# Optimization experiments

Hardware: AMD Instinct MI355X
Metric: run time of the kernel (lower is better)

Reference implementation:

```python
import jax, jax.numpy as jnp
from jax import lax
import numpy as np

N, L, C, G, K = 8, 4096, 256, 8, 3
GC = C // G
DILATION = 1
OFFSET_SCALE = 1.0
LN_EPS = 1e-6


def setup_inputs() -> dict:
    key = jax.random.key(0)
    ks = jax.random.split(key, 14)
    s = lambda k, shp, sc: jax.random.normal(k, shp, jnp.float32) * sc
    return {
        "x": jax.random.normal(ks[0], (N, L, C), jnp.float32),
        "W_in": s(ks[1], (C, C), (1.0 / C) ** 0.5),      # input_proj (in,out)
        "b_in": jnp.zeros((C,), jnp.float32),
        "conv_w": s(ks[2], (C, 1, K), 0.2),              # depthwise conv (O, I/g, K)
        "conv_b": jnp.zeros((C,), jnp.float32),
        "ln_g": jnp.ones((C,), jnp.float32),
        "ln_b": jnp.zeros((C,), jnp.float32),
        "W_off": s(ks[3], (C, G * K), 0.02),             # offset_linear
        "b_off": s(ks[4], (G * K,), 0.02),
        "W_mask": s(ks[5], (C, G * K), 0.02),            # mask_linear
        "b_mask": s(ks[6], (G * K,), 0.02),
        "W_out": s(ks[7], (C, C), (1.0 / C) ** 0.5),     # output_proj
        "b_out": jnp.zeros((C,), jnp.float32),
    }


def _dcnv3_1d(x, W_in, b_in, conv_w, conv_b, ln_g, ln_b,
              W_off, b_off, W_mask, b_mask, W_out, b_out):
    # x: (N, L, C)
    x_proj = x @ W_in + b_in                                     # (N,L,C)

    # depthwise conv -> LayerNorm(C) -> GELU  (the offset/mask feature branch)
    xc = x.transpose(0, 2, 1)                                    # (N,C,L)
    pad = (K - 1) // 2
    y = lax.conv_general_dilated(
        xc, conv_w, window_strides=(1,), padding=[(pad, pad)],
        dimension_numbers=("NCH", "OIH", "NCH"), feature_group_count=C)
    y = y + conv_b[None, :, None]
    y = y.transpose(0, 2, 1)                                     # (N,L,C)
    mu = y.mean(-1, keepdims=True)
    var = ((y - mu) ** 2).mean(-1, keepdims=True)
    y = (y - mu) * lax.rsqrt(var + LN_EPS) * ln_g + ln_b
    x_feat = jax.nn.gelu(y, approximate=False)                   # torch GELU = exact erf

    offset = (x_feat @ W_off + b_off).reshape(N, L, G, K)
    mask = jax.nn.softmax((x_feat @ W_mask + b_mask).reshape(N, L, G, K), axis=-1)

    # sampling locations (grid_sample with align_corners=True unnormalizes back to loc)
    ref_p = jnp.arange(L, dtype=jnp.float32)                     # (L,)
    lo = float(-((K - 1) // 2))
    hi = float((K - 1) // 2)
    dil_grid = jnp.linspace(lo, hi, K) * DILATION                # (K,)
    loc = ref_p[None, :, None, None] + dil_grid[None, None, None, :] \
          + offset * OFFSET_SCALE                                # (N,L,G,K)
    loc = jnp.remainder(loc, L)                                  # in [0, L)

    # bilinear sample along L with zero padding (matches F.grid_sample, H=1)
    f0 = jnp.floor(loc)
    w1 = loc - f0
    w0 = 1.0 - w1
    i0 = jnp.clip(f0.astype(jnp.int32), 0, L - 1)
    i1 = i0 + 1
    valid1 = (i1 < L)
    i1c = jnp.where(valid1, i1, 0)

    x_g = x_proj.reshape(N, L, G, GC)                            # (N,L,G,gc)
    nidx = jnp.arange(N)[:, None, None, None]
    gidx = jnp.arange(G)[None, None, :, None]
    v0 = x_g[nidx, i0, gidx]                                     # (N,L,G,K,gc)
    v1 = x_g[nidx, i1c, gidx] * valid1[..., None].astype(x_g.dtype)
    sampled = w0[..., None] * v0 + w1[..., None] * v1            # (N,L,G,K,gc)

    out = (sampled * mask[..., None]).sum(axis=3)                # (N,L,G,gc)
    out = out.reshape(N, L, C)
    return out @ W_out + b_out


def reference(x, W_in, b_in, conv_w, conv_b, ln_g, ln_b,
              W_off, b_off, W_mask, b_mask, W_out, b_out):
    return _dcnv3_1d(x, W_in, b_in, conv_w, conv_b, ln_g, ln_b,
                     W_off, b_off, W_mask, b_mask, W_out, b_out)
```

## Files before the change

kernel.cpp:

```cpp
#include <hip/hip_runtime.h>
#include <math.h>

constexpr int LL = 4096;
constexpr int CC = 256;
constexpr int MM = 32768;

typedef unsigned int u32;
typedef unsigned short u16;
typedef __attribute__((ext_vector_type(8))) short bf16x8;
typedef __attribute__((ext_vector_type(4))) float f32x4;

__device__ __forceinline__ u16 f2b(float f) {
    u32 u = __float_as_uint(f);
    u32 r = (u + 0x7fffu + ((u >> 16) & 1u)) >> 16;
    return (u16)r;
}

__device__ __forceinline__ void gl_lds16(const u16* g, u16* l) {
    __builtin_amdgcn_global_load_lds(
        (const __attribute__((address_space(1))) unsigned int*)g,
        (__attribute__((address_space(3))) unsigned int*)l, 16, 0, 0);
}

__global__ __launch_bounds__(256) void prep_w(
    const float* __restrict__ W_in, const float* __restrict__ W_out,
    const float* __restrict__ W_off, const float* __restrict__ W_mask,
    u16* __restrict__ Wt_in, u16* __restrict__ Wt_out, u16* __restrict__ Wcomb)
{
    const int b = blockIdx.x, t = threadIdx.x;
    if (b < 256) {
        Wt_in[b * 256 + t]  = f2b(W_in[t * 256 + b]);
        Wt_out[b * 256 + t] = f2b(W_out[t * 256 + b]);
    } else {
        const int j = b - 256;
        const float v = (j < 24) ? W_off[t * 24 + j] : W_mask[t * 24 + (j - 24)];
        Wcomb[j * 256 + t] = f2b(v);
    }
}

__global__ __launch_bounds__(256) void conv_ln_gelu(
    const float* __restrict__ x, const float* __restrict__ cw,
    const float* __restrict__ cbias, const float* __restrict__ lng,
    const float* __restrict__ lnb, u16* __restrict__ xf, u16* __restrict__ xb16)
{
    const int wave = threadIdx.x >> 6;
    const int lane = threadIdx.x & 63;
    const int nl = (blockIdx.x << 2) + wave;
    const int l = nl & (LL - 1);
    const int c0 = lane << 2;
    const size_t base = (size_t)nl * CC + c0;

    float4 xc = *(const float4*)&x[base];
    float4 xm = make_float4(0.f, 0.f, 0.f, 0.f);
    float4 xp = make_float4(0.f, 0.f, 0.f, 0.f);
    if (l > 0)      xm = *(const float4*)&x[base - CC];
    if (l < LL - 1) xp = *(const float4*)&x[base + CC];

    ushort4 xbv;
    xbv.x = f2b(xc.x); xbv.y = f2b(xc.y); xbv.z = f2b(xc.z); xbv.w = f2b(xc.w);
    *(ushort4*)&xb16[base] = xbv;

    float xmv[4] = {xm.x, xm.y, xm.z, xm.w};
    float xcv[4] = {xc.x, xc.y, xc.z, xc.w};
    float xpv[4] = {xp.x, xp.y, xp.z, xp.w};

    float y[4];
    float sum = 0.f, sq = 0.f;
#pragma unroll
    for (int j = 0; j < 4; ++j) {
        const int c = c0 + j;
        float v = fmaf(xmv[j], cw[c * 3 + 0],
                  fmaf(xcv[j], cw[c * 3 + 1],
                  fmaf(xpv[j], cw[c * 3 + 2], cbias[c])));
        y[j] = v;
        sum += v;
        sq  += v * v;
    }
#pragma unroll
    for (int off = 32; off > 0; off >>= 1) {
        sum += __shfl_xor(sum, off);
        sq  += __shfl_xor(sq, off);
    }
    const float mu  = sum * (1.f / CC);
    const float var = sq * (1.f / CC) - mu * mu;
    const float rs  = rsqrtf(var + 1e-6f);

    ushort4 o;
    float ov[4];
#pragma unroll
    for (int j = 0; j < 4; ++j) {
        const int c = c0 + j;
        const float tn = (y[j] - mu) * rs * lng[c] + lnb[c];
        ov[j] = 0.5f * tn * (1.f + erff(tn * 0.70710678118654752f));
    }
    o.x = f2b(ov[0]); o.y = f2b(ov[1]); o.z = f2b(ov[2]); o.w = f2b(ov[3]);
    *(ushort4*)&xf[base] = o;
}

__global__ __launch_bounds__(256, 3) void gemm1(
    const u16* __restrict__ xb, const u16* __restrict__ Wt_in,
    const float* __restrict__ b_in, u16* __restrict__ xprojb)
{
    __shared__ u16 As[2][128 * 32];
    __shared__ u16 Bs[2][128 * 32];

    const int t = threadIdx.x;
    const int w = t >> 6, lane = t & 63;
    const int lr = lane & 15, lk = lane >> 4;
    const int wm = w >> 1, wn = w & 1;

    const int d = blockIdx.x;
    const int m_t = (d & 7) * 32 + (d >> 4);
    const int n_t = (d >> 3) & 1;
    const int m0 = m_t * 128, n0 = n_t * 128;

    const int srow = lane >> 2;
    const int scol = (lane & 3) * 8;

    f32x4 acc[4][4];
#pragma unroll
    for (int i = 0; i < 4; ++i)
#pragma unroll
        for (int j = 0; j < 4; ++j) acc[i][j] = f32x4{0.f, 0.f, 0.f, 0.f};

    auto STAGE = [&](int buf, int kt) {
        const int k0 = kt * 32;
#pragma unroll
        for (int j = 0; j < 2; ++j) {
            const int rr = (w * 2 + j) * 16 + srow;
            u16* ldsbase_a = &As[buf][0] + (w * 2 + j) * 512;
            u16* ldsbase_b = &Bs[buf][0] + (w * 2 + j) * 512;
            gl_lds16(xb    + ((size_t)(m0 + rr) << 8) + k0 + scol, ldsbase_a);
            gl_lds16(Wt_in + ((size_t)(n0 + rr) << 8) + k0 + scol, ldsbase_b);
        }
    };

    STAGE(0, 0);
    for (int kt = 0; kt < 8; ++kt) {
        const int cur = kt & 1;
        __syncthreads();
        if (kt < 7) STAGE(cur ^ 1, kt + 1);
        bf16x8 af[4], bfr[4];
#pragma unroll
        for (int mt = 0; mt < 4; ++mt)
            af[mt] = *(const bf16x8*)&As[cur][(wm * 64 + mt * 16 + lr) * 32 + lk * 8];
#pragma unroll
        for (int nt = 0; nt < 4; ++nt)
            bfr[nt] = *(const bf16x8*)&Bs[cur][(wn * 64 + nt * 16 + lr) * 32 + lk * 8];
#pragma unroll
        for (int mt = 0; mt < 4; ++mt)
#pragma unroll
            for (int nt = 0; nt < 4; ++nt)
                acc[mt][nt] = __builtin_amdgcn_mfma_f32_16x16x32_bf16(
                    af[mt], bfr[nt], acc[mt][nt], 0, 0, 0);
    }

    const int r0 = lk * 4;
#pragma unroll
    for (int nt = 0; nt < 4; ++nt) {
        const int cn = n0 + wn * 64 + nt * 16 + lr;
        const float bv = b_in[cn];
#pragma unroll
        for (int mt = 0; mt < 4; ++mt)
#pragma unroll
            for (int r4 = 0; r4 < 4; ++r4)
                xprojb[(size_t)(m0 + wm * 64 + mt * 16 + r0 + r4) * 256 + cn] =
                    f2b(acc[mt][nt][r4] + bv);
    }
}

__global__ __launch_bounds__(256, 3) void offmask_gemm(
    const u16* __restrict__ xfeatb, const u16* __restrict__ xprojb,
    const u16* __restrict__ Wcomb, const float* __restrict__ boff,
    const float* __restrict__ bmask, const u16* __restrict__ Wt_out,
    const float* __restrict__ b_out, float* __restrict__ out)
{
    __shared__ __align__(16) char s_mem[32768];
    __shared__ uint2 s_pack[512 * 3];
    float* logit = (float*)s_mem;

    const int t = threadIdx.x;
    const int w = t >> 6, lane = t & 63;
    const int lr = lane & 15, lk8 = (lane >> 4) * 8;
    const int r0 = (lane >> 4) * 4;
    const int blk = blockIdx.x;
    const size_t row0 = (size_t)blk * 64;

    f32x4 pacc[3];
#pragma unroll
    for (int ct = 0; ct < 3; ++ct) pacc[ct] = f32x4{0.f, 0.f, 0.f, 0.f};
    const u16* fbase = xfeatb + (row0 + w * 16 + lr) * 256;
#pragma unroll
    for (int ks = 0; ks < 8; ++ks) {
        const int ke = ks * 32 + lk8;
        bf16x8 a = *(const bf16x8*)(fbase + ke);
#pragma unroll
        for (int ct = 0; ct < 3; ++ct) {
            bf16x8 bfr = *(const bf16x8*)(Wcomb + (size_t)(ct * 16 + lr) * 256 + ke);
            pacc[ct] = __builtin_amdgcn_mfma_f32_16x16x32_bf16(a, bfr, pacc[ct], 0, 0, 0);
        }
    }
#pragma unroll
    for (int ct = 0; ct < 3; ++ct) {
        const int j = ct * 16 + lr;
        const float bj = (j < 24) ? boff[j] : bmask[j - 24];
#pragma unroll
        for (int r4 = 0; r4 < 4; ++r4)
            logit[(w * 16 + r0 + r4) * 50 + j] = pacc[ct][r4] + bj;
    }
    __syncthreads();

#pragma unroll
    for (int pi = 0; pi < 2; ++pi) {
        const int pp = pi * 256 + t;
        const int rw = pp >> 3, g = pp & 7;
        const float* lp = &logit[rw * 50];
        const float m0v = lp[24 + g * 3 + 0];
        const float m1v = lp[24 + g * 3 + 1];
        const float m2v = lp[24 + g * 3 + 2];
        const float mx = fmaxf(m0v, fmaxf(m1v, m2v));
        const float e0 = expf(m0v - mx), e1 = expf(m1v - mx), e2 = expf(m2v - mx);
        const float inv = 1.f / (e0 + e1 + e2);
        const float msk[3] = {e0 * inv, e1 * inv, e2 * inv};
        const float lf = (float)((blk & 63) * 64 + rw);
#pragma unroll
        for (int k = 0; k < 3; ++k) {
            const float loc = lf + (float)(k - 1) + lp[g * 3 + k];
            float r = fmodf(loc, (float)LL);
            if (r < 0.f) r += (float)LL;
            const float f0 = floorf(r);
            int i0 = (int)f0;
            i0 = i0 < 0 ? 0 : (i0 > LL - 1 ? LL - 1 : i0);
            const int i1 = i0 + 1;
            const float w1 = r - f0;
            const bool valid = (i1 < LL);
            union { u32 uw; _Float16 h[2]; } uh;
            uh.h[0] = (_Float16)(msk[k] * (1.f - w1));
            uh.h[1] = (_Float16)(valid ? msk[k] * w1 : 0.f);
            const u32 ij = (u32)i0 | ((u32)(valid ? i1 : 0) << 16);
            s_pack[pp * 3 + k] = make_uint2(uh.uw, ij);
        }
    }
    __syncthreads();

    {
        const int ig = t >> 6, tc = t & 63;
        const int c0 = tc * 4, g4 = tc >> 3;
        const u16* xpn = xprojb + (size_t)(blk >> 6) * LL * 256;
        const int ibeg = ig * 16;
#pragma unroll 4
        for (int i = ibeg; i < ibeg + 16; ++i) {
            const int bidx = (i * 8 + g4) * 3;
            float v0 = 0.f, v1 = 0.f, v2 = 0.f, v3 = 0.f;
#pragma unroll
            for (int k = 0; k < 3; ++k) {
                const uint2 pk = s_pack[bidx + k];
                union { u32 uw; _Float16 h[2]; } uh; uh.uw = pk.x;
                const float wa = (float)uh.h[0], wb = (float)uh.h[1];
                const int i0 = (int)(pk.y & 0xffffu), i1 = (int)(pk.y >> 16);
                uint2 ua = *(const uint2*)(xpn + (size_t)i0 * 256 + c0);
                uint2 ub = *(const uint2*)(xpn + (size_t)i1 * 256 + c0);
                v0 = fmaf(wa, __uint_as_float(ua.x << 16),
                     fmaf(wb, __uint_as_float(ub.x << 16), v0));
                v1 = fmaf(wa, __uint_as_float(ua.x & 0xffff0000u),
                     fmaf(wb, __uint_as_float(ub.x & 0xffff0000u), v1));
                v2 = fmaf(wa, __uint_as_float(ua.y << 16),
                     fmaf(wb, __uint_as_float(ub.y << 16), v2));
                v3 = fmaf(wa, __uint_as_float(ua.y & 0xffff0000u),
                     fmaf(wb, __uint_as_float(ub.y & 0xffff0000u), v3));
            }
            uint2 wd;
            wd.x = (u32)f2b(v0) | ((u32)f2b(v1) << 16);
            wd.y = (u32)f2b(v2) | ((u32)f2b(v3) << 16);
            const int addr = (i * 512 + tc * 8) ^ ((i & 7) << 4);
            *(uint2*)(s_mem + addr) = wd;
        }
    }
    __syncthreads();

    f32x4 acc[4][4];
#pragma unroll
    for (int i = 0; i < 4; ++i)
#pragma unroll
        for (int j = 0; j < 4; ++j) acc[i][j] = f32x4{0.f, 0.f, 0.f, 0.f};

    const u16* Bw = Wt_out + (size_t)(w * 64) * 256;
#pragma unroll
    for (int ks = 0; ks < 8; ++ks) {
        bf16x8 af[4], bfr[4];
#pragma unroll
        for (int mt = 0; mt < 4; ++mt) {
            const int rm = mt * 16 + lr;
            const int addr = (rm * 512 + ks * 64 + lk8 * 2) ^ ((rm & 7) << 4);
            af[mt] = *(const bf16x8*)(s_mem + addr);
        }
        const int ke = ks * 32 + lk8;
#pragma unroll
        for (int nt = 0; nt < 4; ++nt)
            bfr[nt] = *(const bf16x8*)(Bw + (size_t)(nt * 16 + lr) * 256 + ke);
#pragma unroll
        for (int mt = 0; mt < 4; ++mt)
#pragma unroll
            for (int nt = 0; nt < 4; ++nt)
                acc[mt][nt] = __builtin_amdgcn_mfma_f32_16x16x32_bf16(
                    af[mt], bfr[nt], acc[mt][nt], 0, 0, 0);
    }
#pragma unroll
    for (int nt = 0; nt < 4; ++nt) {
        const int cn = w * 64 + nt * 16 + lr;
        const float bv = b_out[cn];
#pragma unroll
        for (int mt = 0; mt < 4; ++mt)
#pragma unroll
            for (int r4 = 0; r4 < 4; ++r4)
                out[(row0 + mt * 16 + r0 + r4) * 256 + cn] = acc[mt][nt][r4] + bv;
    }
}

extern "C" void kernel_launch(void* const* d_in, const int* in_sizes, int n_in,
                              void* d_out, int out_size, void* d_ws, size_t ws_size,
                              hipStream_t stream)
{
    const float* x      = (const float*)d_in[0];
    const float* W_in   = (const float*)d_in[1];
    const float* b_in   = (const float*)d_in[2];
    const float* conv_w = (const float*)d_in[3];
    const float* conv_b = (const float*)d_in[4];
    const float* ln_g   = (const float*)d_in[5];
    const float* ln_b   = (const float*)d_in[6];
    const float* W_off  = (const float*)d_in[7];
    const float* b_off  = (const float*)d_in[8];
    const float* W_mask = (const float*)d_in[9];
    const float* b_mask = (const float*)d_in[10];
    const float* W_out  = (const float*)d_in[11];
    const float* b_out  = (const float*)d_in[12];

    u16* xfeatb = (u16*)d_ws;
    u16* xprojb = (u16*)((char*)d_ws + 16777216);
    u16* xb16   = (u16*)((char*)d_ws + 33554432);
    char* wsb   = (char*)d_ws + 50331648;
    u16* Wt_in  = (u16*)(wsb);
    u16* Wt_out = (u16*)(wsb + 131072);
    u16* Wcombp = (u16*)(wsb + 262144);

    prep_w<<<304, 256, 0, stream>>>(W_in, W_out, W_off, W_mask, Wt_in, Wt_out, Wcombp);
    conv_ln_gelu<<<MM / 4, 256, 0, stream>>>(x, conv_w, conv_b, ln_g, ln_b,
                                             xfeatb, xb16);
    gemm1<<<512, 256, 0, stream>>>(xb16, Wt_in, b_in, xprojb);
    offmask_gemm<<<512, 256, 0, stream>>>(xfeatb, xprojb, Wcombp, b_off, b_mask,
                                          Wt_out, b_out, (float*)d_out);
}
```

Baseline: 74.91 us.

## Fuse weight prep into conv kernel and convert fp32 x to bf16 inside gemm1

Merges the weight-transpose prep kernel into the conv/LN/GELU launch as extra blocks, which saves one launch. gemm1 now reads fp32 x directly and packs it to bf16 into LDS inside its software pipeline, so the bf16 copy of x is no longer written and re-read. The sampling loop in the final kernel is widened to 16-byte gathers with 8 channels per thread. In exchange, gemm1 reads twice the A bytes through registers instead of async LDS loads, and its launch bound drops to 2 blocks per CU.

```diff
diff --git a/kernel.cpp b/kernel.cpp
--- a/kernel.cpp
+++ b/kernel.cpp
@@ -15,6 +15,9 @@
     u32 r = (u + 0x7fffu + ((u >> 16) & 1u)) >> 16;
     return (u16)r;
 }
+__device__ __forceinline__ u32 pack2(float a, float b) {
+    return (u32)f2b(a) | ((u32)f2b(b) << 16);
+}
 
 __device__ __forceinline__ void gl_lds16(const u16* g, u16* l) {
     __builtin_amdgcn_global_load_lds(
@@ -22,30 +25,32 @@
         (__attribute__((address_space(3))) unsigned int*)l, 16, 0, 0);
 }
 
-__global__ __launch_bounds__(256) void prep_w(
+__global__ __launch_bounds__(256) void conv_prep(
+    const float* __restrict__ x, const float* __restrict__ cw,
+    const float* __restrict__ cbias, const float* __restrict__ lng,
+    const float* __restrict__ lnb, u16* __restrict__ xf,
     const float* __restrict__ W_in, const float* __restrict__ W_out,
     const float* __restrict__ W_off, const float* __restrict__ W_mask,
     u16* __restrict__ Wt_in, u16* __restrict__ Wt_out, u16* __restrict__ Wcomb)
 {
-    const int b = blockIdx.x, t = threadIdx.x;
-    if (b < 256) {
-        Wt_in[b * 256 + t]  = f2b(W_in[t * 256 + b]);
-        Wt_out[b * 256 + t] = f2b(W_out[t * 256 + b]);
-    } else {
-        const int j = b - 256;
-        const float v = (j < 24) ? W_off[t * 24 + j] : W_mask[t * 24 + (j - 24)];
-        Wcomb[j * 256 + t] = f2b(v);
-    }
-}
-
-__global__ __launch_bounds__(256) void conv_ln_gelu(
-    const float* __restrict__ x, const float* __restrict__ cw,
-    const float* __restrict__ cbias, const float* __restrict__ lng,
-    const float* __restrict__ lnb, u16* __restrict__ xf, u16* __restrict__ xb16)
-{
-    const int wave = threadIdx.x >> 6;
-    const int lane = threadIdx.x & 63;
-    const int nl = (blockIdx.x << 2) + wave;
+    const int bid = blockIdx.x;
+    const int t = threadIdx.x;
+    if (bid >= 8192) {
+        const int b = bid - 8192;
+        if (b < 256) {
+            Wt_in[b * 256 + t]  = f2b(W_in[t * 256 + b]);
+            Wt_out[b * 256 + t] = f2b(W_out[t * 256 + b]);
+        } else {
+            const int j = b - 256;
+            const float v = (j < 24) ? W_off[t * 24 + j] : W_mask[t * 24 + (j - 24)];
+            Wcomb[j * 256 + t] = f2b(v);
+        }
+        return;
+    }
+
+    const int wave = t >> 6;
+    const int lane = t & 63;
+    const int nl = (bid << 2) + wave;
     const int l = nl & (LL - 1);
     const int c0 = lane << 2;
     const size_t base = (size_t)nl * CC + c0;
@@ -55,10 +60,6 @@
     float4 xp = make_float4(0.f, 0.f, 0.f, 0.f);
     if (l > 0)      xm = *(const float4*)&x[base - CC];
     if (l < LL - 1) xp = *(const float4*)&x[base + CC];
-
-    ushort4 xbv;
-    xbv.x = f2b(xc.x); xbv.y = f2b(xc.y); xbv.z = f2b(xc.z); xbv.w = f2b(xc.w);
-    *(ushort4*)&xb16[base] = xbv;
 
     float xmv[4] = {xm.x, xm.y, xm.z, xm.w};
     float xcv[4] = {xc.x, xc.y, xc.z, xc.w};
@@ -97,8 +98,8 @@
     *(ushort4*)&xf[base] = o;
 }
 
-__global__ __launch_bounds__(256, 3) void gemm1(
-    const u16* __restrict__ xb, const u16* __restrict__ Wt_in,
+__global__ __launch_bounds__(256, 2) void gemm1(
+    const float* __restrict__ x, const u16* __restrict__ Wt_in,
     const float* __restrict__ b_in, u16* __restrict__ xprojb)
 {
     __shared__ u16 As[2][128 * 32];
@@ -116,6 +117,8 @@
 
     const int srow = lane >> 2;
     const int scol = (lane & 3) * 8;
+    const int arow = t >> 1;
+    const int akh = (t & 1) * 16;
 
     f32x4 acc[4][4];
 #pragma unroll
@@ -123,23 +126,43 @@
 #pragma unroll
         for (int j = 0; j < 4; ++j) acc[i][j] = f32x4{0.f, 0.f, 0.f, 0.f};
 
-    auto STAGE = [&](int buf, int kt) {
+    auto STAGE_B = [&](int buf, int kt) {
         const int k0 = kt * 32;
 #pragma unroll
         for (int j = 0; j < 2; ++j) {
             const int rr = (w * 2 + j) * 16 + srow;
-            u16* ldsbase_a = &As[buf][0] + (w * 2 + j) * 512;
-            u16* ldsbase_b = &Bs[buf][0] + (w * 2 + j) * 512;
-            gl_lds16(xb    + ((size_t)(m0 + rr) << 8) + k0 + scol, ldsbase_a);
-            gl_lds16(Wt_in + ((size_t)(n0 + rr) << 8) + k0 + scol, ldsbase_b);
+            gl_lds16(Wt_in + ((size_t)(n0 + rr) << 8) + k0 + scol,
+                     &Bs[buf][0] + (w * 2 + j) * 512);
         }
     };
-
-    STAGE(0, 0);
+    const float* Abase = x + (size_t)(m0 + arow) * 256 + akh;
+
+    {
+        float4 f0 = *(const float4*)(Abase);
+        float4 f1 = *(const float4*)(Abase + 4);
+        float4 f2 = *(const float4*)(Abase + 8);
+        float4 f3 = *(const float4*)(Abase + 12);
+        STAGE_B(0, 0);
+        u16* dst = &As[0][arow * 32 + akh];
+        ((u32*)dst)[0] = pack2(f0.x, f0.y); ((u32*)dst)[1] = pack2(f0.z, f0.w);
+        ((u32*)dst)[2] = pack2(f1.x, f1.y); ((u32*)dst)[3] = pack2(f1.z, f1.w);
+        ((u32*)dst)[4] = pack2(f2.x, f2.y); ((u32*)dst)[5] = pack2(f2.z, f2.w);
+        ((u32*)dst)[6] = pack2(f3.x, f3.y); ((u32*)dst)[7] = pack2(f3.z, f3.w);
+    }
+
+#pragma unroll
     for (int kt = 0; kt < 8; ++kt) {
         const int cur = kt & 1;
         __syncthreads();
-        if (kt < 7) STAGE(cur ^ 1, kt + 1);
+        float4 f0, f1, f2, f3;
+        if (kt < 7) {
+            const float* ap = Abase + (kt + 1) * 32;
+            f0 = *(const float4*)(ap);
+            f1 = *(const float4*)(ap + 4);
+            f2 = *(const float4*)(ap + 8);
+            f3 = *(const float4*)(ap + 12);
+            STAGE_B(cur ^ 1, kt + 1);
+        }
         bf16x8 af[4], bfr[4];
 #pragma unroll
         for (int mt = 0; mt < 4; ++mt)
@@ -153,6 +176,13 @@
             for (int nt = 0; nt < 4; ++nt)
                 acc[mt][nt] = __builtin_amdgcn_mfma_f32_16x16x32_bf16(
                     af[mt], bfr[nt], acc[mt][nt], 0, 0, 0);
+        if (kt < 7) {
+            u16* dst = &As[cur ^ 1][arow * 32 + akh];
+            ((u32*)dst)[0] = pack2(f0.x, f0.y); ((u32*)dst)[1] = pack2(f0.z, f0.w);
+            ((u32*)dst)[2] = pack2(f1.x, f1.y); ((u32*)dst)[3] = pack2(f1.z, f1.w);
+            ((u32*)dst)[4] = pack2(f2.x, f2.y); ((u32*)dst)[5] = pack2(f2.z, f2.w);
+            ((u32*)dst)[6] = pack2(f3.x, f3.y); ((u32*)dst)[7] = pack2(f3.z, f3.w);
+        }
     }
 
     const int r0 = lk * 4;
@@ -244,36 +274,37 @@
     __syncthreads();
 
     {
-        const int ig = t >> 6, tc = t & 63;
-        const int c0 = tc * 4, g4 = tc >> 3;
+        const int ig = t >> 5, tc = t & 31;
+        const int c0 = tc * 8, g4 = tc >> 2;
         const u16* xpn = xprojb + (size_t)(blk >> 6) * LL * 256;
-        const int ibeg = ig * 16;
-#pragma unroll 4
-        for (int i = ibeg; i < ibeg + 16; ++i) {
+        const int ibeg = ig * 8;
+#pragma unroll 2
+        for (int i = ibeg; i < ibeg + 8; ++i) {
             const int bidx = (i * 8 + g4) * 3;
-            float v0 = 0.f, v1 = 0.f, v2 = 0.f, v3 = 0.f;
+            float v[8] = {0.f, 0.f, 0.f, 0.f, 0.f, 0.f, 0.f, 0.f};
 #pragma unroll
             for (int k = 0; k < 3; ++k) {
                 const uint2 pk = s_pack[bidx + k];
                 union { u32 uw; _Float16 h[2]; } uh; uh.uw = pk.x;
                 const float wa = (float)uh.h[0], wb = (float)uh.h[1];
                 const int i0 = (int)(pk.y & 0xffffu), i1 = (int)(pk.y >> 16);
-                uint2 ua = *(const uint2*)(xpn + (size_t)i0 * 256 + c0);
-                uint2 ub = *(const uint2*)(xpn + (size_t)i1 * 256 + c0);
-                v0 = fmaf(wa, __uint_as_float(ua.x << 16),
-                     fmaf(wb, __uint_as_float(ub.x << 16), v0));
-                v1 = fmaf(wa, __uint_as_float(ua.x & 0xffff0000u),
-                     fmaf(wb, __uint_as_float(ub.x & 0xffff0000u), v1));
-                v2 = fmaf(wa, __uint_as_float(ua.y << 16),
-                     fmaf(wb, __uint_as_float(ub.y << 16), v2));
-                v3 = fmaf(wa, __uint_as_float(ua.y & 0xffff0000u),
-                     fmaf(wb, __uint_as_float(ub.y & 0xffff0000u), v3));
+                uint4 ua = *(const uint4*)(xpn + (size_t)i0 * 256 + c0);
+                uint4 ub = *(const uint4*)(xpn + (size_t)i1 * 256 + c0);
+                const u32 au[4] = {ua.x, ua.y, ua.z, ua.w};
+                const u32 bu[4] = {ub.x, ub.y, ub.z, ub.w};
+#pragma unroll
+                for (int j = 0; j < 4; ++j) {
+                    v[2 * j]     = fmaf(wa, __uint_as_float(au[j] << 16),
+                                   fmaf(wb, __uint_as_float(bu[j] << 16), v[2 * j]));
+                    v[2 * j + 1] = fmaf(wa, __uint_as_float(au[j] & 0xffff0000u),
+                                   fmaf(wb, __uint_as_float(bu[j] & 0xffff0000u), v[2 * j + 1]));
+                }
             }
-            uint2 wd;
-            wd.x = (u32)f2b(v0) | ((u32)f2b(v1) << 16);
-            wd.y = (u32)f2b(v2) | ((u32)f2b(v3) << 16);
-            const int addr = (i * 512 + tc * 8) ^ ((i & 7) << 4);
-            *(uint2*)(s_mem + addr) = wd;
+            uint4 wd;
+            wd.x = pack2(v[0], v[1]); wd.y = pack2(v[2], v[3]);
+            wd.z = pack2(v[4], v[5]); wd.w = pack2(v[6], v[7]);
+            const int addr = (i * 512 + tc * 16) ^ ((i & 7) << 4);
+            *(uint4*)(s_mem + addr) = wd;
         }
     }
     __syncthreads();
@@ -337,16 +368,15 @@
 
     u16* xfeatb = (u16*)d_ws;
     u16* xprojb = (u16*)((char*)d_ws + 16777216);
-    u16* xb16   = (u16*)((char*)d_ws + 33554432);
-    char* wsb   = (char*)d_ws + 50331648;
+    char* wsb   = (char*)d_ws + 33554432;
     u16* Wt_in  = (u16*)(wsb);
     u16* Wt_out = (u16*)(wsb + 131072);
     u16* Wcombp = (u16*)(wsb + 262144);
 
-    prep_w<<<304, 256, 0, stream>>>(W_in, W_out, W_off, W_mask, Wt_in, Wt_out, Wcombp);
-    conv_ln_gelu<<<MM / 4, 256, 0, stream>>>(x, conv_w, conv_b, ln_g, ln_b,
-                                             xfeatb, xb16);
-    gemm1<<<512, 256, 0, stream>>>(xb16, Wt_in, b_in, xprojb);
+    conv_prep<<<8192 + 304, 256, 0, stream>>>(x, conv_w, conv_b, ln_g, ln_b, xfeatb,
+                                              W_in, W_out, W_off, W_mask,
+                                              Wt_in, Wt_out, Wcombp);
+    gemm1<<<512, 256, 0, stream>>>(x, Wt_in, b_in, xprojb);
     offmask_gemm<<<512, 256, 0, stream>>>(xfeatb, xprojb, Wcombp, b_off, b_mask,
                                           Wt_out, b_out, (float*)d_out);
 }
```

New measurement: 72.04 us. 1.04x faster.
